# Optimization experiments

Measured on AMD Instinct MI355X. Metric: run time of the kernel, lower is better.

## Reference

```python
import jax, jax.numpy as jnp
import numpy as np

B, T, IN, OUT = 4, 2048, 4096, 11008


def setup_inputs() -> dict:
    key = jax.random.key(0)
    k1, k2, k3, k4 = jax.random.split(key, 4)
    x = jax.random.normal(k1, (B, T, IN), dtype=jnp.float32)
    # int8 weight values in [-127, 127]; stored as int32 for harness dtype support
    weight_int8 = jax.random.randint(k2, (OUT, IN), -127, 128, dtype=jnp.int32)
    # per-output-channel scales, positive and small like absmax/127
    weight_scale = jax.random.uniform(k3, (OUT, 1), dtype=jnp.float32, minval=1e-4, maxval=0.02)
    bias = jax.random.normal(k4, (OUT,), dtype=jnp.float32) * 0.01
    return {"x": x, "weight_int8": weight_int8, "weight_scale": weight_scale, "bias": bias}


def reference(x, weight_int8, weight_scale, bias):
    # dequantize: [OUT, IN] float weight = int8 * per-row scale
    weight_fp = weight_int8.astype(jnp.float32) * weight_scale
    weight_fp = weight_fp.astype(x.dtype)
    # F.linear: x @ W^T + b -> [B, T, OUT]
    out = jnp.einsum('bti,oi->bto', x, weight_fp) + bias
    return out
```

## Files before the change

kernel.cpp:

```cpp
#include <hip/hip_runtime.h>
#include <hip/hip_bf16.h>

#define MDIM 8192
#define NDIM 11008
#define KDIM 4096

#define BM 256
#define BN 256
#define BK 64
#define NT (KDIM / BK)

typedef __attribute__((ext_vector_type(4))) int   int4v;
typedef __attribute__((ext_vector_type(4))) float f32x4;


__global__ __launch_bounds__(256) void quant_x_kernel(const float* __restrict__ x,
                                                      int* __restrict__ q,
                                                      float* __restrict__ xs) {
  int row = blockIdx.x;
  int tid = threadIdx.x;
  const float4* xr = (const float4*)(x + (size_t)row * KDIM);
  float4 v[4];
  float amax = 0.f;
#pragma unroll
  for (int i = 0; i < 4; ++i) {
    v[i] = xr[tid + i * 256];
    amax = fmaxf(amax, fmaxf(fmaxf(fabsf(v[i].x), fabsf(v[i].y)),
                             fmaxf(fabsf(v[i].z), fabsf(v[i].w))));
  }
#pragma unroll
  for (int off = 32; off; off >>= 1)
    amax = fmaxf(amax, __shfl_xor(amax, off));
  __shared__ float smax[4];
  if ((tid & 63) == 0) smax[tid >> 6] = amax;
  __syncthreads();
  amax = fmaxf(fmaxf(smax[0], smax[1]), fmaxf(smax[2], smax[3]));
  amax = fmaxf(amax, 1e-20f);
  float inv = 127.f / amax;
  if (tid == 0) xs[row] = amax * (1.f / 127.f);
  int* qr = q + (size_t)row * (KDIM / 4);
#pragma unroll
  for (int i = 0; i < 4; ++i) {
    int a = (int)rintf(v[i].x * inv) & 255;
    int b = (int)rintf(v[i].y * inv) & 255;
    int c = (int)rintf(v[i].z * inv) & 255;
    int d = (int)rintf(v[i].w * inv);
    qr[tid + i * 256] = a | (b << 8) | (c << 16) | (d << 24);
  }
}


__global__ void cvt_w_kernel(const int* __restrict__ w, int* __restrict__ q, int n) {
  int stride = gridDim.x * blockDim.x;
  for (int i = blockIdx.x * blockDim.x + threadIdx.x; i < n; i += stride) {
    int4v v = *(const int4v*)(w + (size_t)i * 4);
    q[i] = (v.x & 255) | ((v.y & 255) << 8) | ((v.z & 255) << 16) | (v.w << 24);
  }
}


#define SBARR() __builtin_amdgcn_sched_barrier(0)
#define BARR()  __builtin_amdgcn_s_barrier()
#define VMW_(n) asm volatile("s_waitcnt vmcnt(" #n ")" ::: "memory")
#define VMW(n)  VMW_(n)

#define GLL(SRC, DST) \
  __builtin_amdgcn_global_load_lds( \
      (const __attribute__((address_space(1))) void*)(SRC), \
      (__attribute__((address_space(3))) void*)(DST), 16, 0, 0)

#define STAGE(GSRC, LBASE, BUFI, T) do { \
    const char* _s = (GSRC) + (T) * 64; \
    GLL(_s, (LBASE) + (BUFI) * 16384 + w * 1024); \
    GLL(_s + rstep, (LBASE) + (BUFI) * 16384 + w * 1024 + 8192); \
  } while (0)

#define RD(LB, BUFI, ROW) \
  (*(const int4v*)((LB) + (BUFI) * 16384 + (ROW) * 64 + kbs))

#define MFMA16(AF, MOFF) do { \
    _Pragma("unroll") for (int mi = 0; mi < 4; ++mi) \
    _Pragma("unroll") for (int ni = 0; ni < 4; ++ni) \
      acc[(MOFF) + mi][ni] = __builtin_amdgcn_mfma_i32_16x16x64_i8( \
          af[mi], bf[ni], acc[(MOFF) + mi][ni], 0, 0, 0); \
  } while (0)

#define KT(T, B_, SD, VN, TAIL) do { \
    _Pragma("unroll") for (int ni = 0; ni < 4; ++ni) bf[ni] = RD(ldsB, B_, brow0 + ni * 16); \
    _Pragma("unroll") for (int mi = 0; mi < 4; ++mi) af[mi] = RD(ldsA, B_, arow0 + mi * 16); \
    if (SD) STAGE(gAs, ldsA, ((B_) + 2) & 3, (T) + 2); \
    SBARR(); \
    __builtin_amdgcn_s_setprio(1); MFMA16(af, 0); __builtin_amdgcn_s_setprio(0); \
    SBARR(); \
    _Pragma("unroll") for (int mi = 0; mi < 4; ++mi) af[mi] = RD(ldsA, B_, arow0 + 64 + mi * 16); \
    if (SD) STAGE(gBs, ldsB, ((B_) + 2) & 3, (T) + 2); \
    SBARR(); \
    __builtin_amdgcn_s_setprio(1); MFMA16(af, 4); __builtin_amdgcn_s_setprio(0); \
    SBARR(); \
    if (!(TAIL)) { VMW(VN); BARR(); SBARR(); } \
  } while (0)

__global__ __launch_bounds__(512, 2) void gemm_i8_kernel(
    const char* __restrict__ A,
    const char* __restrict__ Bt,
    const float* __restrict__ xs,
    const float* __restrict__ scale,
    const float* __restrict__ bias,
    float* __restrict__ C)
{
  __shared__ __attribute__((aligned(16))) char As[4][256][64];
  __shared__ __attribute__((aligned(16))) char Bs[4][256][64];

  const int nbc = NDIM / BN;
  int bid = blockIdx.x;
  int cpx = gridDim.x >> 3;
  int swz = (bid & 7) * cpx + (bid >> 3);
  int brow = (swz / nbc) * BM;
  int bcol = (swz % nbc) * BN;

  int tid  = threadIdx.x;
  int lane = tid & 63;
  int w    = tid >> 6;
  int wr   = (w >> 2) & 1;
  int wc   = w & 3;

  int ra = lane & 15;
  int kb = (lane >> 4) * 16;
  int kbs = kb ^ (((ra >> 1) & 3) << 4);

  int arow0 = wr * 128 + ra;
  int brow0 = wc * 64 + ra;

  int srow = w * 16 + (lane >> 2);
  int csrc = (lane & 3) ^ ((lane >> 3) & 3);
  const char* gAs = A  + (size_t)(brow + srow) * KDIM + csrc * 16;
  const char* gBs = Bt + (size_t)(bcol + srow) * KDIM + csrc * 16;
  const size_t rstep = (size_t)128 * KDIM;

  char* ldsA = &As[0][0][0];
  char* ldsB = &Bs[0][0][0];

  int4v acc[8][4] = {};
  int4v af[4], bf[4];

  STAGE(gAs, ldsA, 0, 0);  STAGE(gBs, ldsB, 0, 0);
  STAGE(gAs, ldsA, 1, 1);  STAGE(gBs, ldsB, 1, 1);
  VMW(4); BARR(); SBARR();

  for (int t = 0; t < 56; t += 4) {
    KT(t,     0, 1, 4, 0);
    KT(t + 1, 1, 1, 4, 0);
    KT(t + 2, 2, 1, 4, 0);
    KT(t + 3, 3, 1, 4, 0);
  }
  KT(56, 0, 1, 4, 0);
  KT(57, 1, 1, 4, 0);
  KT(58, 2, 1, 4, 0);
  KT(59, 3, 1, 4, 0);
  KT(60, 0, 1, 4, 0);
  KT(61, 1, 1, 4, 0);
  KT(62, 2, 0, 0, 0);
  KT(63, 3, 0, 0, 1);

  int col0 = bcol + wc * 64 + ra;
  int row0 = brow + wr * 128 + (lane >> 4) * 4;
  float xr_[8][4];
#pragma unroll
  for (int m = 0; m < 8; ++m)
#pragma unroll
    for (int j = 0; j < 4; ++j)
      xr_[m][j] = xs[row0 + m * 16 + j];
#pragma unroll
  for (int n = 0; n < 4; ++n) {
    int ng = col0 + n * 16;
    float sc = scale[ng];
    float bi = bias[ng];
#pragma unroll
    for (int m = 0; m < 8; ++m) {
      int rg = row0 + m * 16;
#pragma unroll
      for (int j = 0; j < 4; ++j)
        __builtin_nontemporal_store((float)acc[m][n][j] * (xr_[m][j] * sc) + bi,
                                    &C[(size_t)(rg + j) * NDIM + ng]);
    }
  }
}


__global__ void naive_kernel(const float* __restrict__ x, const int* __restrict__ w,
                             const float* __restrict__ scale, const float* __restrict__ bias,
                             float* __restrict__ out)
{
  int n = blockIdx.x * blockDim.x + threadIdx.x;
  int m = blockIdx.y;
  if (n >= NDIM) return;
  const float* xr = x + (size_t)m * KDIM;
  const int* wrow = w + (size_t)n * KDIM;
  float s = 0.f;
  for (int k = 0; k < KDIM; ++k) s += xr[k] * (float)wrow[k];
  out[(size_t)m * NDIM + n] = s * scale[n] + bias[n];
}


extern "C" void kernel_launch(void* const* d_in, const int* in_sizes, int n_in,
                              void* d_out, int out_size, void* d_ws, size_t ws_size,
                              hipStream_t stream) {
  const float* x      = (const float*)d_in[0];
  const int*   w8     = (const int*)d_in[1];
  const float* wscale = (const float*)d_in[2];
  const float* bias   = (const float*)d_in[3];
  float* out = (float*)d_out;

  size_t aq = (size_t)MDIM * KDIM;
  size_t bq = (size_t)NDIM * KDIM;
  size_t xb = (size_t)MDIM * 4;

  if (ws_size >= aq + bq + xb) {
    char* Aq = (char*)d_ws;
    char* Bq = (char*)d_ws + aq;
    float* xsp = (float*)((char*)d_ws + aq + bq);
    quant_x_kernel<<<MDIM, 256, 0, stream>>>(x, (int*)Aq, xsp);
    cvt_w_kernel<<<2048, 256, 0, stream>>>(w8, (int*)Bq, NDIM * KDIM / 4);
    gemm_i8_kernel<<<(MDIM / BM) * (NDIM / BN), 512, 0, stream>>>(
        Aq, Bq, xsp, wscale, bias, out);
  } else {
    naive_kernel<<<dim3((NDIM + 255) / 256, MDIM), 256, 0, stream>>>(x, w8, wscale, bias, out);
  }
}
```

Before: 466.6 us.

## Double-buffer MFMA fragments in registers and deepen global prefetch to three stages

Restructures the int8 GEMM main loop so LDS fragments for the next k-tile are read into a second register set while the current tile's MFMAs run, alternating even and odd fragment sets. Global-to-LDS staging is moved from two to three tiles ahead across the four LDS buffers, with the prologue and tail adjusted to match. The aim is to hide LDS read latency and global load latency behind matrix math. The cost is more live vector registers, which risks spills or lower occupancy under the 512x2 launch bound.

```diff
diff --git a/kernel.cpp b/kernel.cpp
--- a/kernel.cpp
+++ b/kernel.cpp
@@ -10,8 +10,7 @@
 #define BK 64
 #define NT (KDIM / BK)
 
-typedef __attribute__((ext_vector_type(4))) int   int4v;
-typedef __attribute__((ext_vector_type(4))) float f32x4;
+typedef __attribute__((ext_vector_type(4))) int int4v;
 
 
 __global__ __launch_bounds__(256) void quant_x_kernel(const float* __restrict__ x,
@@ -78,26 +77,33 @@
 #define RD(LB, BUFI, ROW) \
   (*(const int4v*)((LB) + (BUFI) * 16384 + (ROW) * 64 + kbs))
 
-#define MFMA16(AF, MOFF) do { \
+#define MFMA16(AF, BF, MOFF) do { \
     _Pragma("unroll") for (int mi = 0; mi < 4; ++mi) \
     _Pragma("unroll") for (int ni = 0; ni < 4; ++ni) \
       acc[(MOFF) + mi][ni] = __builtin_amdgcn_mfma_i32_16x16x64_i8( \
-          af[mi], bf[ni], acc[(MOFF) + mi][ni], 0, 0, 0); \
+          AF[mi], BF[ni], acc[(MOFF) + mi][ni], 0, 0, 0); \
   } while (0)
 
-#define KT(T, B_, SD, VN, TAIL) do { \
-    _Pragma("unroll") for (int ni = 0; ni < 4; ++ni) bf[ni] = RD(ldsB, B_, brow0 + ni * 16); \
-    _Pragma("unroll") for (int mi = 0; mi < 4; ++mi) af[mi] = RD(ldsA, B_, arow0 + mi * 16); \
-    if (SD) STAGE(gAs, ldsA, ((B_) + 2) & 3, (T) + 2); \
-    SBARR(); \
-    __builtin_amdgcn_s_setprio(1); MFMA16(af, 0); __builtin_amdgcn_s_setprio(0); \
-    SBARR(); \
-    _Pragma("unroll") for (int mi = 0; mi < 4; ++mi) af[mi] = RD(ldsA, B_, arow0 + 64 + mi * 16); \
-    if (SD) STAGE(gBs, ldsB, ((B_) + 2) & 3, (T) + 2); \
-    SBARR(); \
-    __builtin_amdgcn_s_setprio(1); MFMA16(af, 4); __builtin_amdgcn_s_setprio(0); \
-    SBARR(); \
-    if (!(TAIL)) { VMW(VN); BARR(); SBARR(); } \
+#define KT(T, SLT, CA, CA2, CB, NA, NA2, NB, SD, EN, PF, LASTT) do { \
+    if (PF) { \
+      _Pragma("unroll") for (int mi = 0; mi < 4; ++mi) \
+        NA2[mi] = RD(ldsA, ((SLT) + 1) & 3, arow0 + 64 + mi * 16); \
+    } \
+    if (SD) STAGE(gAs, ldsA, ((SLT) + 3) & 3, (T) + 3); \
+    SBARR(); \
+    __builtin_amdgcn_s_setprio(1); MFMA16(CA, CB, 0); __builtin_amdgcn_s_setprio(0); \
+    SBARR(); \
+    if (PF) { \
+      _Pragma("unroll") for (int mi = 0; mi < 4; ++mi) \
+        NA[mi] = RD(ldsA, ((SLT) + 1) & 3, arow0 + mi * 16); \
+      _Pragma("unroll") for (int ni = 0; ni < 4; ++ni) \
+        NB[ni] = RD(ldsB, ((SLT) + 1) & 3, brow0 + ni * 16); \
+    } \
+    if (SD) STAGE(gBs, ldsB, ((SLT) + 3) & 3, (T) + 3); \
+    SBARR(); \
+    __builtin_amdgcn_s_setprio(1); MFMA16(CA2, CB, 4); __builtin_amdgcn_s_setprio(0); \
+    SBARR(); \
+    if (!(LASTT)) { VMW(EN); BARR(); SBARR(); } \
   } while (0)
 
 __global__ __launch_bounds__(512, 2) void gemm_i8_kernel(
@@ -141,26 +147,31 @@
   char* ldsB = &Bs[0][0][0];
 
   int4v acc[8][4] = {};
-  int4v af[4], bf[4];
+  int4v afE[4], af2E[4], bfE[4];
+  int4v afO[4], af2O[4], bfO[4];
 
   STAGE(gAs, ldsA, 0, 0);  STAGE(gBs, ldsB, 0, 0);
   STAGE(gAs, ldsA, 1, 1);  STAGE(gBs, ldsB, 1, 1);
+  STAGE(gAs, ldsA, 2, 2);  STAGE(gBs, ldsB, 2, 2);
   VMW(4); BARR(); SBARR();
 
-  for (int t = 0; t < 56; t += 4) {
-    KT(t,     0, 1, 4, 0);
-    KT(t + 1, 1, 1, 4, 0);
-    KT(t + 2, 2, 1, 4, 0);
-    KT(t + 3, 3, 1, 4, 0);
-  }
-  KT(56, 0, 1, 4, 0);
-  KT(57, 1, 1, 4, 0);
-  KT(58, 2, 1, 4, 0);
-  KT(59, 3, 1, 4, 0);
-  KT(60, 0, 1, 4, 0);
-  KT(61, 1, 1, 4, 0);
-  KT(62, 2, 0, 0, 0);
-  KT(63, 3, 0, 0, 1);
+#pragma unroll
+  for (int mi = 0; mi < 4; ++mi) afE[mi]  = RD(ldsA, 0, arow0 + mi * 16);
+#pragma unroll
+  for (int mi = 0; mi < 4; ++mi) af2E[mi] = RD(ldsA, 0, arow0 + 64 + mi * 16);
+#pragma unroll
+  for (int ni = 0; ni < 4; ++ni) bfE[ni]  = RD(ldsB, 0, brow0 + ni * 16);
+
+  for (int t = 0; t < 60; t += 4) {
+    KT(t,     0, afE, af2E, bfE, afO, af2O, bfO, 1, 4, 1, 0);
+    KT(t + 1, 1, afO, af2O, bfO, afE, af2E, bfE, 1, 4, 1, 0);
+    KT(t + 2, 2, afE, af2E, bfE, afO, af2O, bfO, 1, 4, 1, 0);
+    KT(t + 3, 3, afO, af2O, bfO, afE, af2E, bfE, 1, 4, 1, 0);
+  }
+  KT(60, 0, afE, af2E, bfE, afO, af2O, bfO, 1, 4, 1, 0);
+  KT(61, 1, afO, af2O, bfO, afE, af2E, bfE, 0, 0, 1, 0);
+  KT(62, 2, afE, af2E, bfE, afO, af2O, bfO, 0, 0, 1, 0);
+  KT(63, 3, afO, af2O, bfO, afE, af2E, bfE, 0, 0, 0, 1);
 
   int col0 = bcol + wc * 64 + ra;
   int row0 = brow + wr * 128 + (lane >> 4) * 4;
```

Measured after the change: 492.0 us. +5.4%, slower.
